# Optimization experiments

Measured on AMD Instinct MI355X. Metric: run time of the kernel, lower is better.

## Reference

```python
import jax, jax.numpy as jnp
import numpy as np
from jax import lax

LOW_T = 25.0    # int(0.1 * 255)
HIGH_T = 76.0   # int(0.3 * 255)
HYST_ITERS = 64 # cap on hysteresis propagation sweeps
TG22 = 0.4142135623730951  # tan(22.5 deg)
TG67 = 2.414213562373095   # tan(67.5 deg)

SOBEL_X = jnp.array([[-1., 0., 1.], [-2., 0., 2.], [-1., 0., 1.]], dtype=jnp.float32)
SOBEL_Y = jnp.array([[-1., -2., -1.], [0., 0., 0.], [1., 2., 1.]], dtype=jnp.float32)


def _conv3(x, k):
    # x: [B,H,W]; reflect-101 border like cv2.Sobel default
    xp = jnp.pad(x, ((0, 0), (1, 1), (1, 1)), mode='reflect')
    return lax.conv_general_dilated(xp[:, None], k[None, None], (1, 1), 'VALID')[:, 0]


def _dilate3x3(m):
    # 3x3 max-pool (8-connected dilation); m is nonnegative float 0/1
    return lax.reduce_window(m, jnp.float32(0.0), lax.max, (1, 3, 3), (1, 1, 1), 'SAME')


def canny_edge(image, low, high):
    """Batched Canny. image: [B,C,H,W] in [0,1] -> edges [B,1,H,W] in {0,1}."""
    image = lax.stop_gradient(image)  # mirrors .cpu().detach().numpy()
    B, C, H, W = image.shape
    if C == 3:
        gray = 0.299 * image[:, 0] + 0.587 * image[:, 1] + 0.114 * image[:, 2]
    else:
        gray = image[:, 0]
    # (img*255).astype(np.uint8) == floor toward zero for values in [0,1]
    g = jnp.clip(jnp.floor(gray * 255.0), 0.0, 255.0)

    gx = _conv3(g, SOBEL_X)
    gy = _conv3(g, SOBEL_Y)
    mag = jnp.abs(gx) + jnp.abs(gy)  # cv2 default L2gradient=False -> L1 magnitude

    # --- non-maximum suppression (OpenCV-style direction quantization) ---
    mp = jnp.pad(mag, ((0, 0), (1, 1), (1, 1)))

    def sh(dy, dx):
        return mp[:, 1 + dy:1 + dy + H, 1 + dx:1 + dx + W]

    ax, ay = jnp.abs(gx), jnp.abs(gy)
    horiz = ay <= TG22 * ax              # gradient ~horizontal: compare L/R
    vert = ay >= TG67 * ax               # gradient ~vertical: compare U/D
    diag = ~(horiz | vert)
    same_sign = (gx * gy) >= 0
    d1 = diag & same_sign                # 45 deg diagonal

    keep_h = (mag > sh(0, -1)) & (mag >= sh(0, 1))
    keep_v = (mag > sh(-1, 0)) & (mag >= sh(1, 0))
    keep_d1 = (mag > sh(-1, -1)) & (mag >= sh(1, 1))
    keep_d2 = (mag > sh(-1, 1)) & (mag >= sh(1, -1))
    keep = jnp.where(horiz, keep_h,
           jnp.where(vert, keep_v,
           jnp.where(d1, keep_d1, keep_d2)))
    nms = jnp.where(keep, mag, 0.0)

    # --- double threshold + hysteresis (iterative 8-connected propagation) ---
    weak = (nms > low).astype(jnp.float32)
    strong = (nms > high).astype(jnp.float32)

    def cond(state):
        cur, prev, i = state
        return jnp.logical_and(i < HYST_ITERS, jnp.any(cur != prev))

    def body(state):
        cur, prev, i = state
        new = jnp.minimum(_dilate3x3(cur), weak)          # grow strong into weak
        new = jnp.maximum(new, strong)
        return new, cur, i + 1

    edges, _, _ = lax.while_loop(cond, body, (strong, -jnp.ones_like(strong), 0))
    return edges[:, None]  # [B,1,H,W]


def reference(image_A, image_B):
    image_A = jnp.where(image_A.max() > 1, image_A / 2.0, image_A)
    image_B = jnp.where(image_B.max() > 1, image_B / 2.0, image_B)
    edges_A = canny_edge(image_A, LOW_T, HIGH_T)
    edges_B = canny_edge(image_B, LOW_T, HIGH_T)
    diff = edges_A - edges_B
    return jnp.sqrt(jnp.sum(diff * diff))  # Frobenius norm over all elements


def setup_inputs() -> dict:
    key = jax.random.key(0)
    kA, kB = jax.random.split(key)
    image_A = jax.random.uniform(kA, (32, 3, 512, 512), dtype=jnp.float32)
    image_B = jax.random.uniform(kB, (32, 3, 512, 512), dtype=jnp.float32)
    return {"image_A": image_A, "image_B": image_B}
```

## Files before the change

### kernel.cpp

```cpp
#include <hip/hip_runtime.h>
#include <cstdint>

typedef unsigned long long u64;

__device__ __forceinline__ int reflect_row(int t) {
    return t < 0 ? -t : (t > 511 ? 1022 - t : t);
}

__global__ __launch_bounds__(256, 6) void canny_stream(
    const float* __restrict__ imgA, const float* __restrict__ imgB,
    u64* __restrict__ strong_out, u64* __restrict__ weak_out)
{
    const int img  = blockIdx.z;
    const int lane = threadIdx.x & 63;
    const int W    = blockIdx.x * 4 + (threadIdx.x >> 6);
    const int col  = W * 64 + lane;
    const int y0   = blockIdx.y * 32;
    const float* src = (img < 32) ? imgA + (size_t)img * 786432
                                  : imgB + (size_t)(img - 32) * 786432;
    const bool leftEdge = (W == 0), rightEdge = (W == 7);
    const bool lane0 = (lane == 0), lane63 = (lane == 63);
    int hcol = (lane < 2) ? (W * 64 - 2 + lane)
             : (lane >= 62) ? (W * 64 + 64 + (lane - 62)) : col;
    hcol = min(max(hcol, 0), 511);

    float s0=0,s1=0,s2=0,d0=0,d1=0,d2=0;
    float sh0=0,sh1=0,sh2=0,dh0=0,dh1=0,dh2=0;
    float m0=0,m1=0,m2=0,mh0=0,mh1=0,mh2=0;
    float gx1=0,gy1=0,gx2=0,gy2=0;

    int rr = reflect_row(y0 - 2);
    const float* p = src + (size_t)rr * 512;
    float pr = p[col],  pg = p[262144 + col],  pb = p[524288 + col];
    float qr = p[hcol], qg = p[262144 + hcol], qb = p[524288 + hcol];

    for (int t = y0 - 2; t <= y0 + 33; ++t) {
        float cr=pr, cg=pg, cb=pb, hr=qr, hg=qg, hb=qb;
        rr = reflect_row(t + 1);
        p = src + (size_t)rr * 512;
        pr = p[col];  pg = p[262144 + col];  pb = p[524288 + col];
        qr = p[hcol]; qg = p[262144 + hcol]; qb = p[524288 + hcol];

        float gv = fminf(fmaxf(floorf((0.299f*cr + 0.587f*cg + 0.114f*cb) * 255.0f), 0.0f), 255.0f);
        float hv = fminf(fmaxf(floorf((0.299f*hr + 0.587f*hg + 0.114f*hb) * 255.0f), 0.0f), 255.0f);

        float gl  = __shfl_up(gv, 1);
        float grr = __shfl_down(gv, 1);
        float h0  = __shfl(hv, 0),  h1  = __shfl(hv, 1);
        float h62 = __shfl(hv, 62), h63 = __shfl(hv, 63);
        if (lane0)  gl  = leftEdge  ? grr : h1;
        if (lane63) grr = rightEdge ? gl  : h62;

        s0=s1; s1=s2; d0=d1; d1=d2;
        s2 = gl + 2.0f*gv + grr;  d2 = grr - gl;
        sh0=sh1; sh1=sh2; dh0=dh1; dh1=dh2;
        sh2 = lane0 ? (h0 + 2.0f*h1 + gv) : (gv + 2.0f*h62 + h63);
        dh2 = lane0 ? (gv - h0)           : (h63 - gv);

        float gx = d0 + 2.0f*d1 + d2;
        float gy = s2 - s0;
        float mnew = fabsf(gx) + fabsf(gy);
        float gxh = dh0 + 2.0f*dh1 + dh2;
        float gyh = sh2 - sh0;
        float mhnew = fabsf(gxh) + fabsf(gyh);
        bool rowOK = (unsigned)(t - 1) < 512u;
        if (!rowOK) { mnew = 0.0f; mhnew = 0.0f; }
        if ((lane0 && leftEdge) || (lane63 && rightEdge)) mhnew = 0.0f;
        gx1 = gx2; gy1 = gy2; gx2 = gx; gy2 = gy;
        m0=m1; m1=m2; m2=mnew;
        mh0=mh1; mh1=mh2; mh2=mhnew;

        if (t >= y0 + 2) {
            float l0 = lane0  ? mh0 : __shfl_up(m0, 1);
            float l1 = lane0  ? mh1 : __shfl_up(m1, 1);
            float l2 = lane0  ? mh2 : __shfl_up(m2, 1);
            float r0 = lane63 ? mh0 : __shfl_down(m0, 1);
            float r1 = lane63 ? mh1 : __shfl_down(m1, 1);
            float r2 = lane63 ? mh2 : __shfl_down(m2, 1);
            float ax = fabsf(gx1), ay = fabsf(gy1);
            bool horiz = ay <= 0.4142135623730951f * ax;
            bool vert  = ay >= 2.414213562373095f * ax;
            bool dg1   = !(horiz || vert) && (gx1 * gy1 >= 0.0f);
            bool keep = horiz ? (m1 > l1 && m1 >= r1)
                      : vert  ? (m1 > m0 && m1 >= m2)
                      : dg1   ? (m1 > l0 && m1 >= r2)
                              : (m1 > r0 && m1 >= l2);
            float nms = keep ? m1 : 0.0f;
            u64 wweak   = __ballot(nms > 25.0f);
            u64 wstrong = __ballot(nms > 76.0f);
            if (lane0) {
                size_t o = ((size_t)img * 512 + (t - 2)) * 8 + W;
                weak_out[o]   = wweak;
                strong_out[o] = wstrong;
            }
        }
    }
}

__global__ __launch_bounds__(128) void hyst_diff_kernel(
    const u64* __restrict__ strong_in, const u64* __restrict__ weak_in,
    unsigned int* __restrict__ sum, unsigned int* __restrict__ done,
    float* __restrict__ out)
{
    const int pair = blockIdx.z;
    const int ty = blockIdx.y, tx = blockIdx.x;
    const int half = threadIdx.x >> 6;
    const int lane = threadIdx.x & 63;
    const int img = pair + (half ? 32 : 0);

    __shared__ u64 bint[128 * 2];

    const int row0 = ty * 128 - 64;
    const int wc0  = tx * 2 - 1;
    const size_t ibase = (size_t)img * 512 * 8;

    u64 c[4][4], wk[4][4];
    #pragma unroll
    for (int r = 0; r < 4; ++r) {
        int gr = row0 + lane * 4 + r;
        bool rok = (gr >= 0 && gr < 512);
        #pragma unroll
        for (int j = 0; j < 4; ++j) {
            int wc = wc0 + j;
            bool ok = rok && wc >= 0 && wc < 8;
            size_t o = ibase + (size_t)gr * 8 + wc;
            c[r][j]  = ok ? strong_in[o] : 0ULL;
            wk[r][j] = ok ? weak_in[o]   : 0ULL;
        }
    }

    for (int it = 0; it < 64; ++it) {
        u64 h[4][4];
        #pragma unroll
        for (int r = 0; r < 4; ++r) {
            h[r][0] = c[r][0] | (c[r][0] << 1) | (c[r][0] >> 1) | (c[r][1] << 63);
            h[r][1] = c[r][1] | (c[r][1] << 1) | (c[r][1] >> 1) | (c[r][0] >> 63) | (c[r][2] << 63);
            h[r][2] = c[r][2] | (c[r][2] << 1) | (c[r][2] >> 1) | (c[r][1] >> 63) | (c[r][3] << 63);
            h[r][3] = c[r][3] | (c[r][3] << 1) | (c[r][3] >> 1) | (c[r][2] >> 63);
        }
        u64 delta = 0ULL;
        #pragma unroll
        for (int j = 0; j < 4; ++j) {
            u64 top = __shfl_up(h[3][j], 1);
            u64 bot = __shfl_down(h[0][j], 1);
            if (lane == 0)  top = 0ULL;
            if (lane == 63) bot = 0ULL;
            u64 n0 = (h[0][j] | top     | h[1][j]) & wk[0][j];
            u64 n1 = (h[1][j] | h[0][j] | h[2][j]) & wk[1][j];
            u64 n2 = (h[2][j] | h[1][j] | h[3][j]) & wk[2][j];
            u64 n3 = (h[3][j] | h[2][j] | bot    ) & wk[3][j];
            delta |= (n0 ^ c[0][j]) | (n1 ^ c[1][j]) | (n2 ^ c[2][j]) | (n3 ^ c[3][j]);
            c[0][j] = n0; c[1][j] = n1; c[2][j] = n2; c[3][j] = n3;
        }
        if (__ballot(delta != 0ULL) == 0ULL) break;
    }

    if (half == 1 && lane >= 16 && lane < 48) {
        #pragma unroll
        for (int r = 0; r < 4; ++r) {
            int lr = lane * 4 + r - 64;
            bint[lr * 2 + 0] = c[r][1];
            bint[lr * 2 + 1] = c[r][2];
        }
    }
    __syncthreads();

    unsigned int v = 0;
    if (half == 0 && lane >= 16 && lane < 48) {
        #pragma unroll
        for (int r = 0; r < 4; ++r) {
            int lr = lane * 4 + r - 64;
            v += (unsigned int)__popcll(c[r][1] ^ bint[lr * 2 + 0]);
            v += (unsigned int)__popcll(c[r][2] ^ bint[lr * 2 + 1]);
        }
    }
    #pragma unroll
    for (int off = 32; off > 0; off >>= 1) v += __shfl_down(v, off);

    if (threadIdx.x == 0) {
        if (v != 0) atomicAdd(sum, v);
        __threadfence();
        unsigned int ticket = atomicAdd(done, 1);
        if (ticket == 4 * 4 * 32 - 1) {
            __threadfence();
            unsigned int s = atomicAdd(sum, 0u);
            out[0] = sqrtf((float)s);
        }
    }
}

extern "C" void kernel_launch(void* const* d_in, const int* in_sizes, int n_in,
                              void* d_out, int out_size, void* d_ws, size_t ws_size,
                              hipStream_t stream) {
    const float* imgA = (const float*)d_in[0];
    const float* imgB = (const float*)d_in[1];
    float* out = (float*)d_out;
    char* ws = (char*)d_ws;
    u64* strong_m = (u64*)(ws);
    u64* weak_m   = (u64*)(ws + (2u << 20));
    unsigned int* counters = (unsigned int*)(ws + (4u << 20));

    hipMemsetAsync(counters, 0, 2 * sizeof(unsigned int), stream);

    dim3 g1(2, 16, 64);
    canny_stream<<<g1, 256, 0, stream>>>(imgA, imgB, strong_m, weak_m);

    dim3 g2(4, 4, 32);
    hyst_diff_kernel<<<g2, 128, 0, stream>>>(strong_m, weak_m,
                                             counters, counters + 1, out);
}
```

Baseline: 253.8 us.

## Vectorize Canny stage to four pixels per lane with float4 loads

Each lane now processes four adjacent pixels loaded as float4, so a wavefront covers a 256-column strip with 16-row bands instead of 64 columns by 32 rows. Bitmasks are assembled per 16-lane group with xor shuffles rather than ballots. The counter reset moves from a hipMemsetAsync into the first kernel. This cuts load instruction count, vertical halo overhead per column and per-pixel shuffles. In exchange it uses more registers per thread (launch bounds lowered to 4 waves) and re-reads more vertical halo rows because the bands are shorter.

```diff
diff --git a/kernel.cpp b/kernel.cpp
--- a/kernel.cpp
+++ b/kernel.cpp
@@ -7,91 +7,141 @@
     return t < 0 ? -t : (t > 511 ? 1022 - t : t);
 }
 
-__global__ __launch_bounds__(256, 6) void canny_stream(
+__device__ __forceinline__ float gray255(float r, float g, float b) {
+    return fminf(fmaxf(floorf((0.299f * r + 0.587f * g + 0.114f * b) * 255.0f), 0.0f), 255.0f);
+}
+
+__global__ __launch_bounds__(256, 4) void canny_stream4(
     const float* __restrict__ imgA, const float* __restrict__ imgB,
-    u64* __restrict__ strong_out, u64* __restrict__ weak_out)
+    u64* __restrict__ strong_out, u64* __restrict__ weak_out,
+    unsigned int* __restrict__ counters)
 {
-    const int img  = blockIdx.z;
-    const int lane = threadIdx.x & 63;
-    const int W    = blockIdx.x * 4 + (threadIdx.x >> 6);
-    const int col  = W * 64 + lane;
-    const int y0   = blockIdx.y * 32;
+    if (threadIdx.x == 0 && blockIdx.x == 0 && blockIdx.y == 0 && blockIdx.z == 0) {
+        counters[0] = 0u;
+        counters[1] = 0u;
+    }
+    const int img   = blockIdx.z;
+    const int lane  = threadIdx.x & 63;
+    const int wid   = threadIdx.x >> 6;
+    const int strip = blockIdx.x;
+    const int x0    = strip * 256;
+    const int band  = blockIdx.y * 4 + wid;
+    const int y0    = band * 16;
     const float* src = (img < 32) ? imgA + (size_t)img * 786432
                                   : imgB + (size_t)(img - 32) * 786432;
-    const bool leftEdge = (W == 0), rightEdge = (W == 7);
+    const bool leftEdge  = (strip == 0);
+    const bool rightEdge = (strip == 1);
     const bool lane0 = (lane == 0), lane63 = (lane == 63);
-    int hcol = (lane < 2) ? (W * 64 - 2 + lane)
-             : (lane >= 62) ? (W * 64 + 64 + (lane - 62)) : col;
-    hcol = min(max(hcol, 0), 511);
-
-    float s0=0,s1=0,s2=0,d0=0,d1=0,d2=0;
-    float sh0=0,sh1=0,sh2=0,dh0=0,dh1=0,dh2=0;
-    float m0=0,m1=0,m2=0,mh0=0,mh1=0,mh2=0;
-    float gx1=0,gy1=0,gx2=0,gy2=0;
+
+    int hx = lane0 ? x0 - 2 : (lane63 ? x0 + 256 : x0);
+    hx = min(max(hx, 0), 510);
+    const int c4 = (x0 >> 2) + lane;
+
+    float4 z4 = make_float4(0.f, 0.f, 0.f, 0.f);
+    float4 s0 = z4, s1 = z4, s2 = z4, d0 = z4, d1 = z4, d2 = z4;
+    float4 m0 = z4, m1 = z4, m2 = z4;
+    float4 gxA = z4, gyA = z4, gxB = z4, gyB = z4;
+    float sh0 = 0, sh1 = 0, sh2 = 0, dh0 = 0, dh1 = 0, dh2 = 0;
+    float mh0 = 0, mh1 = 0, mh2 = 0;
 
     int rr = reflect_row(y0 - 2);
     const float* p = src + (size_t)rr * 512;
-    float pr = p[col],  pg = p[262144 + col],  pb = p[524288 + col];
-    float qr = p[hcol], qg = p[262144 + hcol], qb = p[524288 + hcol];
-
-    for (int t = y0 - 2; t <= y0 + 33; ++t) {
-        float cr=pr, cg=pg, cb=pb, hr=qr, hg=qg, hb=qb;
+    float4 pr0 = ((const float4*)(p          ))[c4];
+    float4 pr1 = ((const float4*)(p + 262144 ))[c4];
+    float4 pr2 = ((const float4*)(p + 524288 ))[c4];
+    float2 ph0 = *(const float2*)(p + hx);
+    float2 ph1 = *(const float2*)(p + 262144 + hx);
+    float2 ph2 = *(const float2*)(p + 524288 + hx);
+
+    for (int t = y0 - 2; t <= y0 + 17; ++t) {
+        float4 a0 = pr0, a1 = pr1, a2 = pr2;
+        float2 b0 = ph0, b1 = ph1, b2 = ph2;
         rr = reflect_row(t + 1);
         p = src + (size_t)rr * 512;
-        pr = p[col];  pg = p[262144 + col];  pb = p[524288 + col];
-        qr = p[hcol]; qg = p[262144 + hcol]; qb = p[524288 + hcol];
-
-        float gv = fminf(fmaxf(floorf((0.299f*cr + 0.587f*cg + 0.114f*cb) * 255.0f), 0.0f), 255.0f);
-        float hv = fminf(fmaxf(floorf((0.299f*hr + 0.587f*hg + 0.114f*hb) * 255.0f), 0.0f), 255.0f);
-
-        float gl  = __shfl_up(gv, 1);
-        float grr = __shfl_down(gv, 1);
-        float h0  = __shfl(hv, 0),  h1  = __shfl(hv, 1);
-        float h62 = __shfl(hv, 62), h63 = __shfl(hv, 63);
-        if (lane0)  gl  = leftEdge  ? grr : h1;
-        if (lane63) grr = rightEdge ? gl  : h62;
-
-        s0=s1; s1=s2; d0=d1; d1=d2;
-        s2 = gl + 2.0f*gv + grr;  d2 = grr - gl;
-        sh0=sh1; sh1=sh2; dh0=dh1; dh1=dh2;
-        sh2 = lane0 ? (h0 + 2.0f*h1 + gv) : (gv + 2.0f*h62 + h63);
-        dh2 = lane0 ? (gv - h0)           : (h63 - gv);
-
-        float gx = d0 + 2.0f*d1 + d2;
-        float gy = s2 - s0;
-        float mnew = fabsf(gx) + fabsf(gy);
-        float gxh = dh0 + 2.0f*dh1 + dh2;
+        pr0 = ((const float4*)(p          ))[c4];
+        pr1 = ((const float4*)(p + 262144 ))[c4];
+        pr2 = ((const float4*)(p + 524288 ))[c4];
+        ph0 = *(const float2*)(p + hx);
+        ph1 = *(const float2*)(p + 262144 + hx);
+        ph2 = *(const float2*)(p + 524288 + hx);
+
+        float4 g;
+        g.x = gray255(a0.x, a1.x, a2.x);
+        g.y = gray255(a0.y, a1.y, a2.y);
+        g.z = gray255(a0.z, a1.z, a2.z);
+        g.w = gray255(a0.w, a1.w, a2.w);
+        float hga = gray255(b0.x, b1.x, b2.x);
+        float hgb = gray255(b0.y, b1.y, b2.y);
+
+        float gl = __shfl_up(g.w, 1);
+        float gr = __shfl_down(g.x, 1);
+        if (lane0)  gl = leftEdge  ? g.y : hgb;
+        if (lane63) gr = rightEdge ? g.z : hga;
+
+        s0 = s1; s1 = s2; d0 = d1; d1 = d2;
+        s2.x = gl  + 2.f * g.x + g.y;   d2.x = g.y - gl;
+        s2.y = g.x + 2.f * g.y + g.z;   d2.y = g.z - g.x;
+        s2.z = g.y + 2.f * g.z + g.w;   d2.z = g.w - g.y;
+        s2.w = g.z + 2.f * g.w + gr;    d2.w = gr  - g.z;
+        sh0 = sh1; sh1 = sh2; dh0 = dh1; dh1 = dh2;
+        sh2 = lane0 ? (hga + 2.f * hgb + g.x) : (g.w + 2.f * hga + hgb);
+        dh2 = lane0 ? (g.x - hga)             : (hgb - g.w);
+
+        float4 gx, gy, mn;
+        gx.x = d0.x + 2.f * d1.x + d2.x;  gy.x = s2.x - s0.x;  mn.x = fabsf(gx.x) + fabsf(gy.x);
+        gx.y = d0.y + 2.f * d1.y + d2.y;  gy.y = s2.y - s0.y;  mn.y = fabsf(gx.y) + fabsf(gy.y);
+        gx.z = d0.z + 2.f * d1.z + d2.z;  gy.z = s2.z - s0.z;  mn.z = fabsf(gx.z) + fabsf(gy.z);
+        gx.w = d0.w + 2.f * d1.w + d2.w;  gy.w = s2.w - s0.w;  mn.w = fabsf(gx.w) + fabsf(gy.w);
+        float gxh = dh0 + 2.f * dh1 + dh2;
         float gyh = sh2 - sh0;
-        float mhnew = fabsf(gxh) + fabsf(gyh);
-        bool rowOK = (unsigned)(t - 1) < 512u;
-        if (!rowOK) { mnew = 0.0f; mhnew = 0.0f; }
-        if ((lane0 && leftEdge) || (lane63 && rightEdge)) mhnew = 0.0f;
-        gx1 = gx2; gy1 = gy2; gx2 = gx; gy2 = gy;
-        m0=m1; m1=m2; m2=mnew;
-        mh0=mh1; mh1=mh2; mh2=mhnew;
+        float mhn = fabsf(gxh) + fabsf(gyh);
+        if (!((unsigned)(t - 1) < 512u)) { mn = z4; mhn = 0.f; }
+        if ((lane0 && leftEdge) || (lane63 && rightEdge)) mhn = 0.f;
+        m0 = m1; m1 = m2; m2 = mn;
+        mh0 = mh1; mh1 = mh2; mh2 = mhn;
+        gxA = gxB; gyA = gyB; gxB = gx; gyB = gy;
 
         if (t >= y0 + 2) {
-            float l0 = lane0  ? mh0 : __shfl_up(m0, 1);
-            float l1 = lane0  ? mh1 : __shfl_up(m1, 1);
-            float l2 = lane0  ? mh2 : __shfl_up(m2, 1);
-            float r0 = lane63 ? mh0 : __shfl_down(m0, 1);
-            float r1 = lane63 ? mh1 : __shfl_down(m1, 1);
-            float r2 = lane63 ? mh2 : __shfl_down(m2, 1);
-            float ax = fabsf(gx1), ay = fabsf(gy1);
-            bool horiz = ay <= 0.4142135623730951f * ax;
-            bool vert  = ay >= 2.414213562373095f * ax;
-            bool dg1   = !(horiz || vert) && (gx1 * gy1 >= 0.0f);
-            bool keep = horiz ? (m1 > l1 && m1 >= r1)
-                      : vert  ? (m1 > m0 && m1 >= m2)
-                      : dg1   ? (m1 > l0 && m1 >= r2)
-                              : (m1 > r0 && m1 >= l2);
-            float nms = keep ? m1 : 0.0f;
-            u64 wweak   = __ballot(nms > 25.0f);
-            u64 wstrong = __ballot(nms > 76.0f);
-            if (lane0) {
-                size_t o = ((size_t)img * 512 + (t - 2)) * 8 + W;
-                weak_out[o]   = wweak;
-                strong_out[o] = wstrong;
+            float lm0 = lane0  ? mh0 : __shfl_up(m0.w, 1);
+            float lm1 = lane0  ? mh1 : __shfl_up(m1.w, 1);
+            float lm2 = lane0  ? mh2 : __shfl_up(m2.w, 1);
+            float rm0 = lane63 ? mh0 : __shfl_down(m0.x, 1);
+            float rm1 = lane63 ? mh1 : __shfl_down(m1.x, 1);
+            float rm2 = lane63 ? mh2 : __shfl_down(m2.x, 1);
+
+            unsigned nw = 0, ns = 0;
+#define PX(J, C0, C1, C2, L0, L1, L2, R0, R1, R2, GX, GY)                        \
+            {                                                                     \
+                float ax = fabsf(GX), ay = fabsf(GY);                             \
+                bool horiz = ay <= 0.4142135623730951f * ax;                      \
+                bool vert  = ay >= 2.414213562373095f * ax;                       \
+                bool dg1 = !(horiz || vert) && (GX * GY >= 0.0f);                 \
+                bool keep = horiz ? (C1 > L1 && C1 >= R1)                         \
+                          : vert  ? (C1 > C0 && C1 >= C2)                         \
+                          : dg1   ? (C1 > L0 && C1 >= R2)                         \
+                                  : (C1 > R0 && C1 >= L2);                        \
+                float nms = keep ? C1 : 0.0f;                                     \
+                nw |= (nms > 25.0f ? 1u : 0u) << (J);                             \
+                ns |= (nms > 76.0f ? 1u : 0u) << (J);                             \
+            }
+            PX(0, m0.x, m1.x, m2.x, lm0,  lm1,  lm2,  m0.y, m1.y, m2.y, gxA.x, gyA.x)
+            PX(1, m0.y, m1.y, m2.y, m0.x, m1.x, m2.x, m0.z, m1.z, m2.z, gxA.y, gyA.y)
+            PX(2, m0.z, m1.z, m2.z, m0.y, m1.y, m2.y, m0.w, m1.w, m2.w, gxA.z, gyA.z)
+            PX(3, m0.w, m1.w, m2.w, m0.z, m1.z, m2.z, rm0,  rm1,  rm2,  gxA.w, gyA.w)
+#undef PX
+            int sh = (lane & 15) * 4;
+            u64 ww = (u64)nw << sh;
+            u64 ws = (u64)ns << sh;
+            #pragma unroll
+            for (int off = 1; off < 16; off <<= 1) {
+                ww |= __shfl_xor(ww, off, 16);
+                ws |= __shfl_xor(ws, off, 16);
+            }
+            if ((lane & 15) == 0) {
+                int wi = strip * 4 + (lane >> 4);
+                size_t o = ((size_t)img * 512 + (t - 2)) * 8 + wi;
+                weak_out[o]   = ww;
+                strong_out[o] = ws;
             }
         }
     }
@@ -200,10 +250,8 @@
     u64* weak_m   = (u64*)(ws + (2u << 20));
     unsigned int* counters = (unsigned int*)(ws + (4u << 20));
 
-    hipMemsetAsync(counters, 0, 2 * sizeof(unsigned int), stream);
-
-    dim3 g1(2, 16, 64);
-    canny_stream<<<g1, 256, 0, stream>>>(imgA, imgB, strong_m, weak_m);
+    dim3 g1(2, 8, 64);
+    canny_stream4<<<g1, 256, 0, stream>>>(imgA, imgB, strong_m, weak_m, counters);
 
     dim3 g2(4, 4, 32);
     hyst_diff_kernel<<<g2, 128, 0, stream>>>(strong_m, weak_m,
```

New measurement: 246.6 us. -2.8%, faster.

## Rework Canny stage so each wave covers full rows with 8 pixels per lane

Applied to the files above, without the earlier changes.

The first kernel now assigns each wavefront a band of 8 rows across all 512 columns, with each lane processing 8 consecutive pixels loaded as float4 vectors. This removes the per-wave halo columns and the halo shuffles, and packs the NMS bits with xor-shuffles instead of ballots. The vertical halo overhead rises from 4 of 36 rows to 4 of 12 rows per band, and register pressure grows, so occupancy hint drops to 3. The counter memset is folded into the kernel, removing one launch.

```diff
diff --git a/kernel.cpp b/kernel.cpp
--- a/kernel.cpp
+++ b/kernel.cpp
@@ -7,93 +7,133 @@
     return t < 0 ? -t : (t > 511 ? 1022 - t : t);
 }
 
-__global__ __launch_bounds__(256, 6) void canny_stream(
+__device__ __forceinline__ float gray255(float r, float g, float b) {
+    return fminf(fmaxf(floorf((0.299f * r + 0.587f * g + 0.114f * b) * 255.0f), 0.0f), 255.0f);
+}
+
+__global__ __launch_bounds__(256, 3) void canny_row8(
     const float* __restrict__ imgA, const float* __restrict__ imgB,
-    u64* __restrict__ strong_out, u64* __restrict__ weak_out)
+    u64* __restrict__ strong_out, u64* __restrict__ weak_out,
+    unsigned int* __restrict__ counters)
 {
-    const int img  = blockIdx.z;
+    if (threadIdx.x == 0 && blockIdx.x == 0 && blockIdx.y == 0) {
+        counters[0] = 0u;
+        counters[1] = 0u;
+    }
+    const int img  = blockIdx.y;
     const int lane = threadIdx.x & 63;
-    const int W    = blockIdx.x * 4 + (threadIdx.x >> 6);
-    const int col  = W * 64 + lane;
-    const int y0   = blockIdx.y * 32;
-    const float* src = (img < 32) ? imgA + (size_t)img * 786432
-                                  : imgB + (size_t)(img - 32) * 786432;
-    const bool leftEdge = (W == 0), rightEdge = (W == 7);
+    const int band = blockIdx.x * 4 + (threadIdx.x >> 6);
+    const int y0   = band * 8;
+    const float4* src = (const float4*)((img < 32) ? imgA + (size_t)img * 786432
+                                                   : imgB + (size_t)(img - 32) * 786432);
     const bool lane0 = (lane == 0), lane63 = (lane == 63);
-    int hcol = (lane < 2) ? (W * 64 - 2 + lane)
-             : (lane >= 62) ? (W * 64 + 64 + (lane - 62)) : col;
-    hcol = min(max(hcol, 0), 511);
-
-    float s0=0,s1=0,s2=0,d0=0,d1=0,d2=0;
-    float sh0=0,sh1=0,sh2=0,dh0=0,dh1=0,dh2=0;
-    float m0=0,m1=0,m2=0,mh0=0,mh1=0,mh2=0;
-    float gx1=0,gy1=0,gx2=0,gy2=0;
+    const int c4 = lane * 2;
+
+    float s0[8], s1[8], s2[8], d0[8], d1[8], d2[8];
+    float m0[8], m1[8], m2[8], gpx[8], gpy[8];
+    #pragma unroll
+    for (int j = 0; j < 8; ++j) {
+        s0[j] = s1[j] = s2[j] = d0[j] = d1[j] = d2[j] = 0.f;
+        m0[j] = m1[j] = m2[j] = gpx[j] = gpy[j] = 0.f;
+    }
 
     int rr = reflect_row(y0 - 2);
-    const float* p = src + (size_t)rr * 512;
-    float pr = p[col],  pg = p[262144 + col],  pb = p[524288 + col];
-    float qr = p[hcol], qg = p[262144 + hcol], qb = p[524288 + hcol];
-
-    for (int t = y0 - 2; t <= y0 + 33; ++t) {
-        float cr=pr, cg=pg, cb=pb, hr=qr, hg=qg, hb=qb;
+    const float4* q = src + (size_t)rr * 128;
+    float4 pA0 = q[c4],          pA1 = q[c4 + 1];
+    float4 pB0 = q[65536 + c4],  pB1 = q[65536 + c4 + 1];
+    float4 pC0 = q[131072 + c4], pC1 = q[131072 + c4 + 1];
+
+    #pragma unroll
+    for (int k = 0; k < 12; ++k) {
+        const int t = y0 - 2 + k;
+        float4 a0 = pA0, a1 = pA1, b0 = pB0, b1 = pB1, e0 = pC0, e1 = pC1;
         rr = reflect_row(t + 1);
-        p = src + (size_t)rr * 512;
-        pr = p[col];  pg = p[262144 + col];  pb = p[524288 + col];
-        qr = p[hcol]; qg = p[262144 + hcol]; qb = p[524288 + hcol];
-
-        float gv = fminf(fmaxf(floorf((0.299f*cr + 0.587f*cg + 0.114f*cb) * 255.0f), 0.0f), 255.0f);
-        float hv = fminf(fmaxf(floorf((0.299f*hr + 0.587f*hg + 0.114f*hb) * 255.0f), 0.0f), 255.0f);
-
-        float gl  = __shfl_up(gv, 1);
-        float grr = __shfl_down(gv, 1);
-        float h0  = __shfl(hv, 0),  h1  = __shfl(hv, 1);
-        float h62 = __shfl(hv, 62), h63 = __shfl(hv, 63);
-        if (lane0)  gl  = leftEdge  ? grr : h1;
-        if (lane63) grr = rightEdge ? gl  : h62;
-
-        s0=s1; s1=s2; d0=d1; d1=d2;
-        s2 = gl + 2.0f*gv + grr;  d2 = grr - gl;
-        sh0=sh1; sh1=sh2; dh0=dh1; dh1=dh2;
-        sh2 = lane0 ? (h0 + 2.0f*h1 + gv) : (gv + 2.0f*h62 + h63);
-        dh2 = lane0 ? (gv - h0)           : (h63 - gv);
-
-        float gx = d0 + 2.0f*d1 + d2;
-        float gy = s2 - s0;
-        float mnew = fabsf(gx) + fabsf(gy);
-        float gxh = dh0 + 2.0f*dh1 + dh2;
-        float gyh = sh2 - sh0;
-        float mhnew = fabsf(gxh) + fabsf(gyh);
-        bool rowOK = (unsigned)(t - 1) < 512u;
-        if (!rowOK) { mnew = 0.0f; mhnew = 0.0f; }
-        if ((lane0 && leftEdge) || (lane63 && rightEdge)) mhnew = 0.0f;
-        gx1 = gx2; gy1 = gy2; gx2 = gx; gy2 = gy;
-        m0=m1; m1=m2; m2=mnew;
-        mh0=mh1; mh1=mh2; mh2=mhnew;
-
-        if (t >= y0 + 2) {
-            float l0 = lane0  ? mh0 : __shfl_up(m0, 1);
-            float l1 = lane0  ? mh1 : __shfl_up(m1, 1);
-            float l2 = lane0  ? mh2 : __shfl_up(m2, 1);
-            float r0 = lane63 ? mh0 : __shfl_down(m0, 1);
-            float r1 = lane63 ? mh1 : __shfl_down(m1, 1);
-            float r2 = lane63 ? mh2 : __shfl_down(m2, 1);
-            float ax = fabsf(gx1), ay = fabsf(gy1);
-            bool horiz = ay <= 0.4142135623730951f * ax;
-            bool vert  = ay >= 2.414213562373095f * ax;
-            bool dg1   = !(horiz || vert) && (gx1 * gy1 >= 0.0f);
-            bool keep = horiz ? (m1 > l1 && m1 >= r1)
-                      : vert  ? (m1 > m0 && m1 >= m2)
-                      : dg1   ? (m1 > l0 && m1 >= r2)
-                              : (m1 > r0 && m1 >= l2);
-            float nms = keep ? m1 : 0.0f;
-            u64 wweak   = __ballot(nms > 25.0f);
-            u64 wstrong = __ballot(nms > 76.0f);
-            if (lane0) {
-                size_t o = ((size_t)img * 512 + (t - 2)) * 8 + W;
-                weak_out[o]   = wweak;
-                strong_out[o] = wstrong;
+        q = src + (size_t)rr * 128;
+        pA0 = q[c4];          pA1 = q[c4 + 1];
+        pB0 = q[65536 + c4];  pB1 = q[65536 + c4 + 1];
+        pC0 = q[131072 + c4]; pC1 = q[131072 + c4 + 1];
+
+        float g[10];
+        g[1] = gray255(a0.x, b0.x, e0.x);
+        g[2] = gray255(a0.y, b0.y, e0.y);
+        g[3] = gray255(a0.z, b0.z, e0.z);
+        g[4] = gray255(a0.w, b0.w, e0.w);
+        g[5] = gray255(a1.x, b1.x, e1.x);
+        g[6] = gray255(a1.y, b1.y, e1.y);
+        g[7] = gray255(a1.z, b1.z, e1.z);
+        g[8] = gray255(a1.w, b1.w, e1.w);
+        float gl = __shfl_up(g[8], 1);
+        float gr = __shfl_down(g[1], 1);
+        g[0] = lane0  ? g[2] : gl;
+        g[9] = lane63 ? g[7] : gr;
+
+        #pragma unroll
+        for (int j = 0; j < 8; ++j) {
+            float sn = g[j] + 2.f * g[j + 1] + g[j + 2];
+            float dn = g[j + 2] - g[j];
+            s0[j] = s1[j]; s1[j] = s2[j]; s2[j] = sn;
+            d0[j] = d1[j]; d1[j] = d2[j]; d2[j] = dn;
+        }
+
+        const bool rowOK = (unsigned)(t - 1) < 512u;
+        float gxn[8], gyn[8];
+        #pragma unroll
+        for (int j = 0; j < 8; ++j) {
+            float gx = d0[j] + 2.f * d1[j] + d2[j];
+            float gy = s2[j] - s0[j];
+            float mn = rowOK ? (fabsf(gx) + fabsf(gy)) : 0.f;
+            gxn[j] = gx; gyn[j] = gy;
+            m0[j] = m1[j]; m1[j] = m2[j]; m2[j] = mn;
+        }
+
+        if (k >= 4) {
+            float lm0 = __shfl_up(m0[7], 1), lm1 = __shfl_up(m1[7], 1), lm2 = __shfl_up(m2[7], 1);
+            float rm0 = __shfl_down(m0[0], 1), rm1 = __shfl_down(m1[0], 1), rm2 = __shfl_down(m2[0], 1);
+            if (lane0)  { lm0 = 0.f; lm1 = 0.f; lm2 = 0.f; }
+            if (lane63) { rm0 = 0.f; rm1 = 0.f; rm2 = 0.f; }
+
+            unsigned nw = 0, ns = 0;
+#define PX(J, L0, L1, L2, R0, R1, R2)                                             \
+            {                                                                      \
+                float GX = gpx[J], GY = gpy[J];                                    \
+                float ax = fabsf(GX), ay = fabsf(GY);                              \
+                bool horiz = ay <= 0.4142135623730951f * ax;                       \
+                bool vert  = ay >= 2.414213562373095f * ax;                        \
+                bool dg1 = !(horiz || vert) && (GX * GY >= 0.0f);                  \
+                float C0 = m0[J], C1 = m1[J], C2 = m2[J];                          \
+                bool keep = horiz ? (C1 > (L1) && C1 >= (R1))                      \
+                          : vert  ? (C1 > C0 && C1 >= C2)                          \
+                          : dg1   ? (C1 > (L0) && C1 >= (R2))                      \
+                                  : (C1 > (R0) && C1 >= (L2));                     \
+                float nms = keep ? C1 : 0.0f;                                      \
+                nw |= (nms > 25.0f ? 1u : 0u) << (J);                              \
+                ns |= (nms > 76.0f ? 1u : 0u) << (J);                              \
             }
-        }
+            PX(0, lm0,   lm1,   lm2,   m0[1], m1[1], m2[1])
+            PX(1, m0[0], m1[0], m2[0], m0[2], m1[2], m2[2])
+            PX(2, m0[1], m1[1], m2[1], m0[3], m1[3], m2[3])
+            PX(3, m0[2], m1[2], m2[2], m0[4], m1[4], m2[4])
+            PX(4, m0[3], m1[3], m2[3], m0[5], m1[5], m2[5])
+            PX(5, m0[4], m1[4], m2[4], m0[6], m1[6], m2[6])
+            PX(6, m0[5], m1[5], m2[5], m0[7], m1[7], m2[7])
+            PX(7, m0[6], m1[6], m2[6], rm0,   rm1,   rm2  )
+#undef PX
+            int sh = (lane & 7) * 8;
+            u64 ww = (u64)nw << sh;
+            u64 ws = (u64)ns << sh;
+            #pragma unroll
+            for (int off = 1; off < 8; off <<= 1) {
+                ww |= __shfl_xor(ww, off, 8);
+                ws |= __shfl_xor(ws, off, 8);
+            }
+            if ((lane & 7) == 0) {
+                size_t o = ((size_t)img * 512 + (t - 2)) * 8 + (lane >> 3);
+                weak_out[o]   = ww;
+                strong_out[o] = ws;
+            }
+        }
+        #pragma unroll
+        for (int j = 0; j < 8; ++j) { gpx[j] = gxn[j]; gpy[j] = gyn[j]; }
     }
 }
 
@@ -200,10 +240,8 @@
     u64* weak_m   = (u64*)(ws + (2u << 20));
     unsigned int* counters = (unsigned int*)(ws + (4u << 20));
 
-    hipMemsetAsync(counters, 0, 2 * sizeof(unsigned int), stream);
-
-    dim3 g1(2, 16, 64);
-    canny_stream<<<g1, 256, 0, stream>>>(imgA, imgB, strong_m, weak_m);
+    dim3 g1(16, 64);
+    canny_row8<<<g1, 256, 0, stream>>>(imgA, imgB, strong_m, weak_m, counters);
 
     dim3 g2(4, 4, 32);
     hyst_diff_kernel<<<g2, 128, 0, stream>>>(strong_m, weak_m,
```

Result: slower. 297.0 us (+17.0%).
